# Kernel tuning notes

Measured on AMD Instinct MI355X. Metric: run time of the kernel, lower is better.

The kernel has to match this reference:

```python
import jax, jax.numpy as jnp
import numpy as np

B, C, F, T = 4, 64, 257, 256
H, OUT = 256, 64

def setup_inputs() -> dict:
    key = jax.random.key(0)
    ks = jax.random.split(key, 7)
    w = lambda k, shape: jax.random.normal(k, shape, dtype=jnp.float32) * 0.05
    return {
        "x": jax.random.normal(ks[0], (B, C, F, T), dtype=jnp.float32),
        "W_ih": w(ks[1], (4 * H, C)),   # torch LSTM weight_ih_l0, gate order i,f,g,o
        "W_hh": w(ks[2], (4 * H, H)),   # weight_hh_l0
        "b_ih": w(ks[3], (4 * H,)),
        "b_hh": w(ks[4], (4 * H,)),
        "W_lin": w(ks[5], (OUT, H)),
        "b_lin": w(ks[6], (OUT,)),
    }

def _lstm(y, W_ih, W_hh, b_ih, b_hh):
    # y: (N, T, C) -> (N, T, H); PyTorch gate order i, f, g, o
    N, Tl, _ = y.shape
    Hd = W_hh.shape[1]
    # precompute input contributions for all timesteps in one big GEMM
    x_gates = jnp.einsum('ntc,gc->ntg', y, W_ih) + b_ih + b_hh  # (N, T, 4H)

    def step(carry, xg):
        h, c = carry
        g = xg + h @ W_hh.T  # (N, 4H)
        i, f, gg, o = jnp.split(g, 4, axis=-1)
        c = jax.nn.sigmoid(f) * c + jax.nn.sigmoid(i) * jnp.tanh(gg)
        h = jax.nn.sigmoid(o) * jnp.tanh(c)
        return (h, c), h

    h0 = jnp.zeros((N, Hd), y.dtype)
    _, hs = jax.lax.scan(step, (h0, h0), jnp.swapaxes(x_gates, 0, 1))  # (T, N, H)
    return jnp.swapaxes(hs, 0, 1)  # (N, T, H)

def reference(x, W_ih, W_hh, b_ih, b_hh, W_lin, b_lin):
    b, c, f, t = x.shape
    y = x.transpose(0, 2, 3, 1).reshape(b * f, t, c)  # (B*F, T, C)
    h = _lstm(y, W_ih, W_hh, b_ih, b_hh)              # (B*F, T, H)
    out = h @ W_lin.T + b_lin                          # (B*F, T, OUT)
    return out.reshape(b, f, t, -1).transpose(0, 3, 1, 2)  # (B, OUT, F, T)
```

## Files before the change

### kernel.cpp

```cpp
#include <hip/hip_runtime.h>

#define NSEQ 1028
#define TT   256
#define CC   64
#define HH   256
#define SLABE 32768
#define AROWX 528
#define XG_A  (16*AROWX)
#define XG_LDS (2*XG_A + 2*SLABE*2)
#define AROWB 656
#define FB_LDS (2*16*AROWB + 2*SLABE*2)
#define OUTP_LDS (128*264*2 + 64*264*2)

typedef unsigned short u16;
typedef float  f32x4 __attribute__((ext_vector_type(4)));
typedef __bf16 v8bf  __attribute__((ext_vector_type(8)));

__device__ __forceinline__ u16 f2bf(float f){
  unsigned u = __builtin_bit_cast(unsigned, f);
  u += 0x7FFFu + ((u >> 16) & 1u);
  return (u16)(u >> 16);
}
__device__ __forceinline__ float sigm(float x){
  float t = __builtin_amdgcn_exp2f(-1.4426950408889634f * x);
  return __builtin_amdgcn_rcpf(1.0f + t);
}
__device__ __forceinline__ float tanh_f(float x){
  float a = __builtin_fabsf(x);
  float t = __builtin_amdgcn_exp2f(-2.885390081777927f * a);
  float r = (1.0f - t) * __builtin_amdgcn_rcpf(1.0f + t);
  return __builtin_copysignf(r, x);
}
__device__ __forceinline__ void mfma_a(f32x4& d, v8bf a, v8bf b){
  asm("v_mfma_f32_16x16x32_bf16 %0, %1, %2, %0" : "+v"(d) : "v"(a), "a"(b));
}
__device__ __forceinline__ void mfma_v(f32x4& d, v8bf a, v8bf b){
  asm("v_mfma_f32_16x16x32_bf16 %0, %1, %2, %0" : "+v"(d) : "v"(a), "v"(b));
}

__global__ void k_pack_w(const float* __restrict__ Whh, const float* __restrict__ Wih,
                         u16* __restrict__ wpack){
  int idx = blockIdx.x*256 + threadIdx.x;
  if (idx >= 10*SLABE) return;
  int j    = idx & 7;
  int lane = (idx >> 3) & 63;
  int ct   = (idx >> 9) & 7;
  int w    = (idx >> 12) & 7;
  int kt   = idx >> 15;
  int col  = (ct >> 1)*256 + w*32 + (ct & 1)*16 + (lane & 15);
  int k    = kt*32 + (lane >> 4)*8 + j;
  float v  = (k < 256) ? Whh[col*256 + k] : Wih[col*64 + (k - 256)];
  wpack[idx] = f2bf(v);
}

__global__ void k_bias(const float* __restrict__ bi, const float* __restrict__ bh,
                       float* __restrict__ bias){
  int i = blockIdx.x*256 + threadIdx.x;
  if (i < 1024) bias[i] = bi[i] + bh[i];
}

__global__ void k_wlin(const float* __restrict__ Wl, u16* __restrict__ wlin){
  int i = blockIdx.x*256 + threadIdx.x;
  if (i >= 64*264) return;
  int col = i / 264, k = i % 264;
  wlin[i] = (k < 256) ? f2bf(Wl[col*256 + k]) : (u16)0;
}

__global__ void k_ytrans(const float* __restrict__ x, u16* __restrict__ ybuf){
  __shared__ u16 tile[64][257];
  int n = blockIdx.x, b = n / 257, f = n % 257, tid = threadIdx.x;
  for (int i = tid; i < 64*256; i += 256){
    int c = i >> 8, t = i & 255;
    tile[c][t] = f2bf(x[((size_t)(b*64 + c)*257 + f)*256 + t]);
  }
  __syncthreads();
  for (int i = tid; i < 256*64; i += 256){
    int t = i >> 6, c = i & 63;
    ybuf[((size_t)n*256 + t)*64 + c] = tile[c][t];
  }
}

__global__ __launch_bounds__(512) void k_xgates(const u16* __restrict__ wpack,
      const float* __restrict__ bias, const u16* __restrict__ ybuf,
      u16* __restrict__ xgp){
  __shared__ u16 yt[16*16*72];
  const int g = blockIdx.x, t0 = blockIdx.y*16, n0 = g*16;
  const int tid = threadIdx.x, lane = tid & 63, w = tid >> 6;
  const int l15 = lane & 15, q = lane >> 4;

  v8bf wf[2][8];
  #pragma unroll
  for (int kf = 0; kf < 2; ++kf)
    #pragma unroll
    for (int ct = 0; ct < 8; ++ct)
      wf[kf][ct] = *(const v8bf*)(wpack + (((8 + kf)*8 + w)*8 + ct)*512 + lane*8);
  float biasr[8];
  #pragma unroll
  for (int ct = 0; ct < 8; ++ct)
    biasr[ct] = bias[(ct >> 1)*256 + w*32 + (ct & 1)*16 + l15];

  #pragma unroll
  for (int s = 0; s < 4; ++s){
    int i = tid + s*512;
    int seq = i >> 7, tt = (i >> 3) & 15, c8 = i & 7;
    uint4 v = {0u,0u,0u,0u};
    if (n0 + seq < NSEQ)
      v = *(const uint4*)(ybuf + ((size_t)(n0 + seq)*TT + t0 + tt)*64 + c8*8);
    *(uint4*)(yt + tt*1152 + seq*72 + c8*8) = v;
  }
  __syncthreads();

  for (int tt = 0; tt < 16; ++tt){
    f32x4 acc[8];
    #pragma unroll
    for (int ct = 0; ct < 8; ++ct)
      acc[ct] = (f32x4){biasr[ct], biasr[ct], biasr[ct], biasr[ct]};
    v8bf a0 = *(const v8bf*)(yt + tt*1152 + l15*72 + q*8);
    v8bf a1 = *(const v8bf*)(yt + tt*1152 + l15*72 + 32 + q*8);
    #pragma unroll
    for (int ct = 0; ct < 8; ++ct){
      acc[ct] = __builtin_amdgcn_mfma_f32_16x16x32_bf16(a0, wf[0][ct], acc[ct], 0, 0, 0);
      acc[ct] = __builtin_amdgcn_mfma_f32_16x16x32_bf16(a1, wf[1][ct], acc[ct], 0, 0, 0);
    }
    unsigned dw[16];
    #pragma unroll
    for (int ct = 0; ct < 8; ++ct)
      #pragma unroll
      for (int p = 0; p < 2; ++p)
        dw[ct*2 + p] = (unsigned)f2bf(acc[ct][2*p]) | ((unsigned)f2bf(acc[ct][2*p + 1]) << 16);
    u16* dst = xgp + ((((size_t)g*TT + t0 + tt)*8 + w)*64 + lane)*32;
    *(uint4*)(dst +  0) = (uint4){dw[0], dw[1], dw[2], dw[3]};
    *(uint4*)(dst +  8) = (uint4){dw[4], dw[5], dw[6], dw[7]};
    *(uint4*)(dst + 16) = (uint4){dw[8], dw[9], dw[10], dw[11]};
    *(uint4*)(dst + 24) = (uint4){dw[12], dw[13], dw[14], dw[15]};
  }
}

__global__ __launch_bounds__(512, 2) void k_lstm_xg(const u16* __restrict__ wpack,
      const u16* __restrict__ xgp, u16* __restrict__ hbuf){
  extern __shared__ char smem[];
  char* lA = smem;
  u16*  lW = (u16*)(smem + 2*XG_A);
  const int tid = threadIdx.x, lane = tid & 63, w = tid >> 6;
  const int g = blockIdx.x, n0 = g*16;
  const int l15 = lane & 15, q = lane >> 4;
  const int srow = tid >> 5, schunk = tid & 31;

  v8bf wreg[4][8];
  #pragma unroll
  for (int kt = 0; kt < 4; ++kt)
    #pragma unroll
    for (int ct = 0; ct < 8; ++ct)
      wreg[kt][ct] = *(const v8bf*)(wpack + ((kt*8 + w)*8 + ct)*512 + lane*8);

  {
    const uint4* src = (const uint4*)(wpack + 4*SLABE);
    uint4* dst = (uint4*)lW;
    for (int i = tid; i < (2*SLABE)/8; i += 512) dst[i] = src[i];
  }
  {
    unsigned* z = (unsigned*)lA;
    for (int i = tid; i < (2*XG_A)/4; i += 512) z[i] = 0;
  }
  f32x4 creg[2];
  creg[0] = (f32x4){0.f,0.f,0.f,0.f};
  creg[1] = (f32x4){0.f,0.f,0.f,0.f};
  __syncthreads();

  const u16* wp = wpack;

  v8bf sbuf[8];
  uint4 xgv[4];
  {
    const u16* wpw0 = wp + w*4096 + lane*8;
    #pragma unroll
    for (int ct = 0; ct < 8; ++ct) sbuf[ct] = *(const v8bf*)(wpw0 + 6*SLABE + ct*512);
    const u16* xb = xgp + ((((size_t)g*TT + 0)*8 + w)*64 + lane)*32;
    xgv[0] = *(const uint4*)(xb +  0);
    xgv[1] = *(const uint4*)(xb +  8);
    xgv[2] = *(const uint4*)(xb + 16);
    xgv[3] = *(const uint4*)(xb + 24);
  }

  for (int t = 0; t < TT; ++t){
    char* Acur = lA + (t & 1)*XG_A;
    char* Anxt = lA + ((t + 1) & 1)*XG_A;
    asm("" : "+s"(wp));
    const u16* wpw = wp + w*4096 + lane*8;

    if (t >= 1 && n0 + srow < NSEQ){
      uint4 hv = *(const uint4*)(Acur + srow*AROWX + schunk*16);
      *(uint4*)(hbuf + ((size_t)(n0 + srow)*TT + (t - 1))*HH + schunk*8) = hv;
    }

    f32x4 acc[8];
    #pragma unroll
    for (int ct = 0; ct < 8; ++ct){
      #pragma unroll
      for (int p = 0; p < 2; ++p){
        unsigned u = ((const unsigned*)&xgv[(ct*2 + p) >> 2])[(ct*2 + p) & 3];
        acc[ct][2*p]     = __builtin_bit_cast(float, u << 16);
        acc[ct][2*p + 1] = __builtin_bit_cast(float, u & 0xffff0000u);
      }
    }
    asm volatile("s_nop 1"
      : "+v"(acc[0]), "+v"(acc[1]), "+v"(acc[2]), "+v"(acc[3]),
        "+v"(acc[4]), "+v"(acc[5]), "+v"(acc[6]), "+v"(acc[7]));

    if (t + 1 < TT){
      const u16* xb = xgp + ((((size_t)g*TT + (t + 1))*8 + w)*64 + lane)*32;
      xgv[0] = *(const uint4*)(xb +  0);
      xgv[1] = *(const uint4*)(xb +  8);
      xgv[2] = *(const uint4*)(xb + 16);
      xgv[3] = *(const uint4*)(xb + 24);
    }
    __builtin_amdgcn_sched_barrier(0);

    #define AFRAGX(kt) (*(const v8bf*)(Acur + l15*AROWX + (kt)*64 + q*16))
    #define LFRAGX(kt,ct) (*(const v8bf*)(lW + (((kt)-4)*8 + w)*4096 + (ct)*512 + lane*8))

    { v8bf a = AFRAGX(0);
      #pragma unroll
      for (int ct = 0; ct < 8; ++ct) mfma_a(acc[ct], a, wreg[0][ct]); }
    { v8bf a = AFRAGX(6);
      #pragma unroll
      for (int ct = 0; ct < 8; ++ct) mfma_v(acc[ct], a, sbuf[ct]);
      #pragma unroll
      for (int ct = 0; ct < 8; ++ct) sbuf[ct] = *(const v8bf*)(wpw + 7*SLABE + ct*512);
      __builtin_amdgcn_sched_barrier(0); }
    { v8bf a = AFRAGX(1);
      #pragma unroll
      for (int ct = 0; ct < 8; ++ct) mfma_a(acc[ct], a, wreg[1][ct]); }
    { v8bf a = AFRAGX(2);
      #pragma unroll
      for (int ct = 0; ct < 8; ++ct) mfma_a(acc[ct], a, wreg[2][ct]); }
    { v8bf a = AFRAGX(3);
      #pragma unroll
      for (int ct = 0; ct < 8; ++ct) mfma_a(acc[ct], a, wreg[3][ct]); }
    { v8bf a = AFRAGX(4);
      #pragma unroll
      for (int ct = 0; ct < 8; ++ct) mfma_v(acc[ct], a, LFRAGX(4,ct)); }
    { v8bf a = AFRAGX(7);
      #pragma unroll
      for (int ct = 0; ct < 8; ++ct) mfma_v(acc[ct], a, sbuf[ct]);
      #pragma unroll
      for (int ct = 0; ct < 8; ++ct) sbuf[ct] = *(const v8bf*)(wpw + 6*SLABE + ct*512);
      __builtin_amdgcn_sched_barrier(0); }
    { v8bf a = AFRAGX(5);
      #pragma unroll
      for (int ct = 0; ct < 8; ++ct) mfma_v(acc[ct], a, LFRAGX(5,ct)); }

    asm volatile("s_nop 7\n\ts_nop 7\n\ts_nop 7"
      : "+v"(acc[0]), "+v"(acc[1]), "+v"(acc[2]), "+v"(acc[3]),
        "+v"(acc[4]), "+v"(acc[5]), "+v"(acc[6]), "+v"(acc[7]));

    #pragma unroll
    for (int u = 0; u < 2; ++u){
      #pragma unroll
      for (int j = 0; j < 4; ++j){
        float xi = acc[0 + u][j], xf = acc[2 + u][j], xg = acc[4 + u][j], xo = acc[6 + u][j];
        float cv = sigm(xf)*creg[u][j] + sigm(xi)*tanh_f(xg);
        float hv = sigm(xo)*tanh_f(cv);
        creg[u][j] = cv;
        int row = 4*q + j, unit = w*32 + u*16 + l15;
        *(u16*)(Anxt + row*AROWX + unit*2) = f2bf(hv);
      }
    }
    __syncthreads();
  }
  {
    char* Afin = lA + (TT & 1)*XG_A;
    if (n0 + srow < NSEQ){
      uint4 hv = *(const uint4*)(Afin + srow*AROWX + schunk*16);
      *(uint4*)(hbuf + ((size_t)(n0 + srow)*TT + (TT - 1))*HH + schunk*8) = hv;
    }
  }
}

__global__ __launch_bounds__(512, 2) void k_lstm_fb(const u16* __restrict__ wpack,
      const float* __restrict__ bias, const u16* __restrict__ ybuf,
      u16* __restrict__ hbuf){
  extern __shared__ char smem[];
  char* lA = smem;
  u16*  lW = (u16*)(smem + 2*16*AROWB);
  const int tid = threadIdx.x, lane = tid & 63, w = tid >> 6;
  const int n0 = blockIdx.x * 16;
  const int l15 = lane & 15, q = lane >> 4;
  const int srow = tid >> 5, schunk = tid & 31;

  v8bf wreg[4][8];
  #pragma unroll
  for (int kt = 0; kt < 4; ++kt)
    #pragma unroll
    for (int ct = 0; ct < 8; ++ct)
      wreg[kt][ct] = *(const v8bf*)(wpack + ((kt*8 + w)*8 + ct)*512 + lane*8);
  {
    const uint4* src = (const uint4*)(wpack + 4*SLABE);
    uint4* dst = (uint4*)lW;
    for (int i = tid; i < (2*SLABE)/8; i += 512) dst[i] = src[i];
  }
  float biasr[8];
  #pragma unroll
  for (int ct = 0; ct < 8; ++ct)
    biasr[ct] = bias[(ct >> 1)*256 + w*32 + (ct & 1)*16 + l15];
  {
    unsigned* z = (unsigned*)lA;
    for (int i = tid; i < (2*16*AROWB)/4; i += 512) z[i] = 0;
  }
  __syncthreads();
  {
    unsigned v = 0;
    if (n0 + srow < NSEQ)
      v = *(const unsigned*)(ybuf + ((size_t)(n0 + srow)*TT + 0)*64 + (tid & 31)*2);
    *(unsigned*)(lA + srow*AROWB + 512 + (tid & 31)*4) = v;
  }
  f32x4 creg[2];
  creg[0] = (f32x4){0.f,0.f,0.f,0.f};
  creg[1] = (f32x4){0.f,0.f,0.f,0.f};
  __syncthreads();

  const u16* wp = wpack;
  v8bf sbuf[8];
  {
    const u16* wpw0 = wp + w*4096 + lane*8;
    #pragma unroll
    for (int ct = 0; ct < 8; ++ct) sbuf[ct] = *(const v8bf*)(wpw0 + 6*SLABE + ct*512);
  }

  for (int t = 0; t < TT; ++t){
    char* Acur = lA + (t & 1)*16*AROWB;
    char* Anxt = lA + ((t + 1) & 1)*16*AROWB;
    asm("" : "+s"(wp));
    const u16* wpw = wp + w*4096 + lane*8;

    unsigned yv = 0;
    if (t + 1 < TT && n0 + srow < NSEQ)
      yv = *(const unsigned*)(ybuf + ((size_t)(n0 + srow)*TT + (t + 1))*64 + (tid & 31)*2);

    if (t >= 1 && n0 + srow < NSEQ){
      uint4 hv = *(const uint4*)(Acur + srow*AROWB + schunk*16);
      *(uint4*)(hbuf + ((size_t)(n0 + srow)*TT + (t - 1))*HH + schunk*8) = hv;
    }

    f32x4 acc[8];
    #pragma unroll
    for (int ct = 0; ct < 8; ++ct)
      acc[ct] = (f32x4){biasr[ct], biasr[ct], biasr[ct], biasr[ct]};
    asm volatile("s_nop 1"
      : "+v"(acc[0]), "+v"(acc[1]), "+v"(acc[2]), "+v"(acc[3]),
        "+v"(acc[4]), "+v"(acc[5]), "+v"(acc[6]), "+v"(acc[7]));

    #define AFRAG(kt) (*(const v8bf*)(Acur + l15*AROWB + (kt)*64 + q*16))
    #define LFRAG(kt,ct) (*(const v8bf*)(lW + (((kt)-4)*8 + w)*4096 + (ct)*512 + lane*8))

    { v8bf a = AFRAG(0);
      #pragma unroll
      for (int ct = 0; ct < 8; ++ct) mfma_a(acc[ct], a, wreg[0][ct]); }
    { v8bf a = AFRAG(1);
      #pragma unroll
      for (int ct = 0; ct < 8; ++ct) mfma_a(acc[ct], a, wreg[1][ct]); }
    { v8bf a = AFRAG(6);
      #pragma unroll
      for (int ct = 0; ct < 8; ++ct) mfma_v(acc[ct], a, sbuf[ct]);
      #pragma unroll
      for (int ct = 0; ct < 8; ++ct) sbuf[ct] = *(const v8bf*)(wpw + 7*SLABE + ct*512);
      __builtin_amdgcn_sched_barrier(0); }
    { v8bf a = AFRAG(2);
      #pragma unroll
      for (int ct = 0; ct < 8; ++ct) mfma_a(acc[ct], a, wreg[2][ct]); }
    { v8bf a = AFRAG(3);
      #pragma unroll
      for (int ct = 0; ct < 8; ++ct) mfma_a(acc[ct], a, wreg[3][ct]); }
    { v8bf a = AFRAG(7);
      #pragma unroll
      for (int ct = 0; ct < 8; ++ct) mfma_v(acc[ct], a, sbuf[ct]);
      #pragma unroll
      for (int ct = 0; ct < 8; ++ct) sbuf[ct] = *(const v8bf*)(wpw + 8*SLABE + ct*512);
      __builtin_amdgcn_sched_barrier(0); }
    { v8bf a = AFRAG(4);
      #pragma unroll
      for (int ct = 0; ct < 8; ++ct) mfma_v(acc[ct], a, LFRAG(4,ct)); }
    { v8bf a = AFRAG(8);
      #pragma unroll
      for (int ct = 0; ct < 8; ++ct) mfma_v(acc[ct], a, sbuf[ct]);
      #pragma unroll
      for (int ct = 0; ct < 8; ++ct) sbuf[ct] = *(const v8bf*)(wpw + 9*SLABE + ct*512);
      __builtin_amdgcn_sched_barrier(0); }
    { v8bf a = AFRAG(5);
      #pragma unroll
      for (int ct = 0; ct < 8; ++ct) mfma_v(acc[ct], a, LFRAG(5,ct)); }
    { v8bf a = AFRAG(9);
      #pragma unroll
      for (int ct = 0; ct < 8; ++ct) mfma_v(acc[ct], a, sbuf[ct]);
      #pragma unroll
      for (int ct = 0; ct < 8; ++ct) sbuf[ct] = *(const v8bf*)(wpw + 6*SLABE + ct*512);
      __builtin_amdgcn_sched_barrier(0); }

    asm volatile("s_nop 7\n\ts_nop 7\n\ts_nop 7"
      : "+v"(acc[0]), "+v"(acc[1]), "+v"(acc[2]), "+v"(acc[3]),
        "+v"(acc[4]), "+v"(acc[5]), "+v"(acc[6]), "+v"(acc[7]));

    #pragma unroll
    for (int u = 0; u < 2; ++u){
      #pragma unroll
      for (int j = 0; j < 4; ++j){
        float xi = acc[0 + u][j], xf = acc[2 + u][j], xg = acc[4 + u][j], xo = acc[6 + u][j];
        float cv = sigm(xf)*creg[u][j] + sigm(xi)*tanh_f(xg);
        float hv = sigm(xo)*tanh_f(cv);
        creg[u][j] = cv;
        int row = 4*q + j, unit = w*32 + u*16 + l15;
        *(u16*)(Anxt + row*AROWB + unit*2) = f2bf(hv);
      }
    }
    if (t + 1 < TT)
      *(unsigned*)(Anxt + srow*AROWB + 512 + (tid & 31)*4) = yv;
    __syncthreads();
  }
  {
    char* Afin = lA + (TT & 1)*16*AROWB;
    if (n0 + srow < NSEQ){
      uint4 hv = *(const uint4*)(Afin + srow*AROWB + schunk*16);
      *(uint4*)(hbuf + ((size_t)(n0 + srow)*TT + (TT - 1))*HH + schunk*8) = hv;
    }
  }
}

__global__ __launch_bounds__(256) void k_outproj(const u16* __restrict__ hbuf,
      const u16* __restrict__ wlin, const float* __restrict__ blin,
      float* __restrict__ out){
  extern __shared__ char smem[];
  u16* sA = (u16*)smem;
  u16* sB = (u16*)(smem + 128*264*2);
  const int n = blockIdx.x, th = blockIdx.y, t0 = th*128;
  const int b = n / 257, f = n % 257;
  const int tid = threadIdx.x, lane = tid & 63, wv = tid >> 6;

  for (int i = tid; i < 128*32; i += 256){
    int r = i >> 5, part = i & 31;
    *(uint4*)(sA + r*264 + part*8) =
        *(const uint4*)(hbuf + ((size_t)n*TT + t0 + r)*HH + part*8);
  }
  for (int i = tid; i < (64*264)/2; i += 256)
    ((unsigned*)sB)[i] = ((const unsigned*)wlin)[i];
  __syncthreads();

  f32x4 acc[2][4];
  #pragma unroll
  for (int m = 0; m < 2; ++m)
    #pragma unroll
    for (int nt = 0; nt < 4; ++nt){
      float bv = blin[nt*16 + (lane & 15)];
      acc[m][nt] = (f32x4){bv, bv, bv, bv};
    }
  const int khi = (lane >> 4) * 8;
  #pragma unroll
  for (int kt = 0; kt < 8; ++kt){
    v8bf av[2];
    #pragma unroll
    for (int m = 0; m < 2; ++m){
      int mt = wv*2 + m;
      av[m] = *(const v8bf*)(sA + (mt*16 + (lane & 15))*264 + kt*32 + khi);
    }
    #pragma unroll
    for (int nt = 0; nt < 4; ++nt){
      v8bf bv = *(const v8bf*)(sB + (nt*16 + (lane & 15))*264 + kt*32 + khi);
      #pragma unroll
      for (int m = 0; m < 2; ++m)
        acc[m][nt] = __builtin_amdgcn_mfma_f32_16x16x32_bf16(av[m], bv, acc[m][nt], 0, 0, 0);
    }
  }
  #pragma unroll
  for (int m = 0; m < 2; ++m){
    int mt = wv*2 + m;
    #pragma unroll
    for (int nt = 0; nt < 4; ++nt){
      int o = nt*16 + (lane & 15);
      int tb = t0 + mt*16 + 4*(lane >> 4);
      *(f32x4*)(out + (((size_t)b*64 + o)*257 + f)*TT + tb) = acc[m][nt];
    }
  }
}

extern "C" void kernel_launch(void* const* d_in, const int* in_sizes, int n_in,
                              void* d_out, int out_size, void* d_ws, size_t ws_size,
                              hipStream_t stream) {
  const float* x   = (const float*)d_in[0];
  const float* Wih = (const float*)d_in[1];
  const float* Whh = (const float*)d_in[2];
  const float* bih = (const float*)d_in[3];
  const float* bhh = (const float*)d_in[4];
  const float* Wl  = (const float*)d_in[5];
  const float* bl  = (const float*)d_in[6];
  float* out = (float*)d_out;

  char* p = (char*)d_ws;
  u16*   wpack = (u16*)p;   p += 655360;
  float* bias  = (float*)p; p += 4096;
  u16*   wlin  = (u16*)p;   p += 33792;
  u16*   ybuf  = (u16*)p;   p += (size_t)NSEQ*TT*CC*2;
  u16*   hbuf  = (u16*)p;   p += (size_t)NSEQ*TT*HH*2;
  u16*   xgp   = (u16*)p;
  const size_t XGP_BYTES = (size_t)65*TT*8*64*32*2;
  const size_t NEED = (size_t)(p - (char*)d_ws) + XGP_BYTES;

  hipFuncSetAttribute((const void*)k_lstm_xg, hipFuncAttributeMaxDynamicSharedMemorySize, XG_LDS);
  hipFuncSetAttribute((const void*)k_lstm_fb, hipFuncAttributeMaxDynamicSharedMemorySize, FB_LDS);
  hipFuncSetAttribute((const void*)k_outproj, hipFuncAttributeMaxDynamicSharedMemorySize, OUTP_LDS);

  k_pack_w <<<1280, 256, 0, stream>>>(Whh, Wih, wpack);
  k_bias   <<<4,    256, 0, stream>>>(bih, bhh, bias);
  k_wlin   <<<66,   256, 0, stream>>>(Wl, wlin);
  k_ytrans <<<1028, 256, 0, stream>>>(x, ybuf);

  if (ws_size >= NEED) {
    k_xgates <<<dim3(65, 16), 512, 0, stream>>>(wpack, bias, ybuf, xgp);
    k_lstm_xg<<<65, 512, XG_LDS, stream>>>(wpack, xgp, hbuf);
  } else {
    k_lstm_fb<<<65, 512, FB_LDS, stream>>>(wpack, bias, ybuf, hbuf);
  }
  k_outproj<<<dim3(1028, 2), 256, OUTP_LDS, stream>>>(hbuf, wlin, bl, out);
}
```

Baseline: 1.199 ms.

## Chunk LSTM time loop to fit precomputed input gates in workspace

Splits the time dimension into chunks whose size depends on available workspace. Each chunk launches an input-gate GEMM then the recurrent kernel, with hidden and cell state carried across launches via global buffers. This lets the precomputed-input-gates path run when the full buffer doesn't fit, instead of the fallback kernel. It also replaces __syncthreads with an LDS-only wait barrier and reorders MFMA k-tiles. The cost is extra launches and state save/restore per chunk.

```diff
diff --git a/kernel.cpp b/kernel.cpp
--- a/kernel.cpp
+++ b/kernel.cpp
@@ -5,8 +5,8 @@
 #define CC   64
 #define HH   256
 #define SLABE 32768
-#define AROWX 528
-#define XG_A  (16*AROWX)
+#define XROW 528
+#define XG_A (16*XROW)
 #define XG_LDS (2*XG_A + 2*SLABE*2)
 #define AROWB 656
 #define FB_LDS (2*16*AROWB + 2*SLABE*2)
@@ -36,6 +36,12 @@
 }
 __device__ __forceinline__ void mfma_v(f32x4& d, v8bf a, v8bf b){
   asm("v_mfma_f32_16x16x32_bf16 %0, %1, %2, %0" : "+v"(d) : "v"(a), "v"(b));
+}
+__device__ __forceinline__ void soft_barrier(){
+  asm volatile("s_waitcnt lgkmcnt(0)" ::: "memory");
+  __builtin_amdgcn_sched_barrier(0);
+  __builtin_amdgcn_s_barrier();
+  __builtin_amdgcn_sched_barrier(0);
 }
 
 __global__ void k_pack_w(const float* __restrict__ Whh, const float* __restrict__ Wih,
@@ -82,9 +88,9 @@
 
 __global__ __launch_bounds__(512) void k_xgates(const u16* __restrict__ wpack,
       const float* __restrict__ bias, const u16* __restrict__ ybuf,
-      u16* __restrict__ xgp){
+      u16* __restrict__ xgs, int t0, int CH){
   __shared__ u16 yt[16*16*72];
-  const int g = blockIdx.x, t0 = blockIdx.y*16, n0 = g*16;
+  const int g = blockIdx.x, tb = blockIdx.y*16, n0 = g*16;
   const int tid = threadIdx.x, lane = tid & 63, w = tid >> 6;
   const int l15 = lane & 15, q = lane >> 4;
 
@@ -105,7 +111,7 @@
     int seq = i >> 7, tt = (i >> 3) & 15, c8 = i & 7;
     uint4 v = {0u,0u,0u,0u};
     if (n0 + seq < NSEQ)
-      v = *(const uint4*)(ybuf + ((size_t)(n0 + seq)*TT + t0 + tt)*64 + c8*8);
+      v = *(const uint4*)(ybuf + ((size_t)(n0 + seq)*TT + t0 + tb + tt)*64 + c8*8);
     *(uint4*)(yt + tt*1152 + seq*72 + c8*8) = v;
   }
   __syncthreads();
@@ -128,7 +134,7 @@
       #pragma unroll
       for (int p = 0; p < 2; ++p)
         dw[ct*2 + p] = (unsigned)f2bf(acc[ct][2*p]) | ((unsigned)f2bf(acc[ct][2*p + 1]) << 16);
-    u16* dst = xgp + ((((size_t)g*TT + t0 + tt)*8 + w)*64 + lane)*32;
+    u16* dst = xgs + ((((size_t)g*CH + tb + tt)*8 + w)*64 + lane)*32;
     *(uint4*)(dst +  0) = (uint4){dw[0], dw[1], dw[2], dw[3]};
     *(uint4*)(dst +  8) = (uint4){dw[4], dw[5], dw[6], dw[7]};
     *(uint4*)(dst + 16) = (uint4){dw[8], dw[9], dw[10], dw[11]};
@@ -137,7 +143,8 @@
 }
 
 __global__ __launch_bounds__(512, 2) void k_lstm_xg(const u16* __restrict__ wpack,
-      const u16* __restrict__ xgp, u16* __restrict__ hbuf){
+      const u16* __restrict__ xgs, u16* __restrict__ hbuf, float* __restrict__ cbuf,
+      int t0, int CH){
   extern __shared__ char smem[];
   char* lA = smem;
   u16*  lW = (u16*)(smem + 2*XG_A);
@@ -152,19 +159,29 @@
     #pragma unroll
     for (int ct = 0; ct < 8; ++ct)
       wreg[kt][ct] = *(const v8bf*)(wpack + ((kt*8 + w)*8 + ct)*512 + lane*8);
-
   {
     const uint4* src = (const uint4*)(wpack + 4*SLABE);
     uint4* dst = (uint4*)lW;
     for (int i = tid; i < (2*SLABE)/8; i += 512) dst[i] = src[i];
   }
   {
-    unsigned* z = (unsigned*)lA;
-    for (int i = tid; i < (2*XG_A)/4; i += 512) z[i] = 0;
+    uint4 hv = {0u,0u,0u,0u};
+    if (t0 > 0 && n0 + srow < NSEQ)
+      hv = *(const uint4*)(hbuf + ((size_t)(n0 + srow)*TT + (t0 - 1))*HH + schunk*8);
+    *(uint4*)(lA + (t0 & 1)*XG_A + srow*XROW + schunk*16) = hv;
   }
   f32x4 creg[2];
   creg[0] = (f32x4){0.f,0.f,0.f,0.f};
   creg[1] = (f32x4){0.f,0.f,0.f,0.f};
+  if (t0 > 0){
+    #pragma unroll
+    for (int u = 0; u < 2; ++u)
+      #pragma unroll
+      for (int j = 0; j < 4; ++j){
+        int row = 4*q + j, unit = w*32 + u*16 + l15;
+        if (n0 + row < NSEQ) creg[u][j] = cbuf[(size_t)(n0 + row)*HH + unit];
+      }
+  }
   __syncthreads();
 
   const u16* wp = wpack;
@@ -175,21 +192,21 @@
     const u16* wpw0 = wp + w*4096 + lane*8;
     #pragma unroll
     for (int ct = 0; ct < 8; ++ct) sbuf[ct] = *(const v8bf*)(wpw0 + 6*SLABE + ct*512);
-    const u16* xb = xgp + ((((size_t)g*TT + 0)*8 + w)*64 + lane)*32;
+    const u16* xb = xgs + ((((size_t)g*CH + 0)*8 + w)*64 + lane)*32;
     xgv[0] = *(const uint4*)(xb +  0);
     xgv[1] = *(const uint4*)(xb +  8);
     xgv[2] = *(const uint4*)(xb + 16);
     xgv[3] = *(const uint4*)(xb + 24);
   }
 
-  for (int t = 0; t < TT; ++t){
+  for (int t = t0; t < t0 + CH; ++t){
     char* Acur = lA + (t & 1)*XG_A;
     char* Anxt = lA + ((t + 1) & 1)*XG_A;
     asm("" : "+s"(wp));
     const u16* wpw = wp + w*4096 + lane*8;
 
-    if (t >= 1 && n0 + srow < NSEQ){
-      uint4 hv = *(const uint4*)(Acur + srow*AROWX + schunk*16);
+    if (t > t0 && n0 + srow < NSEQ){
+      uint4 hv = *(const uint4*)(Acur + srow*XROW + schunk*16);
       *(uint4*)(hbuf + ((size_t)(n0 + srow)*TT + (t - 1))*HH + schunk*8) = hv;
     }
 
@@ -207,8 +224,8 @@
       : "+v"(acc[0]), "+v"(acc[1]), "+v"(acc[2]), "+v"(acc[3]),
         "+v"(acc[4]), "+v"(acc[5]), "+v"(acc[6]), "+v"(acc[7]));
 
-    if (t + 1 < TT){
-      const u16* xb = xgp + ((((size_t)g*TT + (t + 1))*8 + w)*64 + lane)*32;
+    if (t + 1 < t0 + CH){
+      const u16* xb = xgs + ((((size_t)g*CH + (t + 1 - t0))*8 + w)*64 + lane)*32;
       xgv[0] = *(const uint4*)(xb +  0);
       xgv[1] = *(const uint4*)(xb +  8);
       xgv[2] = *(const uint4*)(xb + 16);
@@ -216,18 +233,18 @@
     }
     __builtin_amdgcn_sched_barrier(0);
 
-    #define AFRAGX(kt) (*(const v8bf*)(Acur + l15*AROWX + (kt)*64 + q*16))
+    #define AFRAGX(kt) (*(const v8bf*)(Acur + l15*XROW + (kt)*64 + q*16))
     #define LFRAGX(kt,ct) (*(const v8bf*)(lW + (((kt)-4)*8 + w)*4096 + (ct)*512 + lane*8))
 
-    { v8bf a = AFRAGX(0);
-      #pragma unroll
-      for (int ct = 0; ct < 8; ++ct) mfma_a(acc[ct], a, wreg[0][ct]); }
     { v8bf a = AFRAGX(6);
       #pragma unroll
       for (int ct = 0; ct < 8; ++ct) mfma_v(acc[ct], a, sbuf[ct]);
       #pragma unroll
       for (int ct = 0; ct < 8; ++ct) sbuf[ct] = *(const v8bf*)(wpw + 7*SLABE + ct*512);
       __builtin_amdgcn_sched_barrier(0); }
+    { v8bf a = AFRAGX(0);
+      #pragma unroll
+      for (int ct = 0; ct < 8; ++ct) mfma_a(acc[ct], a, wreg[0][ct]); }
     { v8bf a = AFRAGX(1);
       #pragma unroll
       for (int ct = 0; ct < 8; ++ct) mfma_a(acc[ct], a, wreg[1][ct]); }
@@ -240,15 +257,15 @@
     { v8bf a = AFRAGX(4);
       #pragma unroll
       for (int ct = 0; ct < 8; ++ct) mfma_v(acc[ct], a, LFRAGX(4,ct)); }
+    { v8bf a = AFRAGX(5);
+      #pragma unroll
+      for (int ct = 0; ct < 8; ++ct) mfma_v(acc[ct], a, LFRAGX(5,ct)); }
     { v8bf a = AFRAGX(7);
       #pragma unroll
       for (int ct = 0; ct < 8; ++ct) mfma_v(acc[ct], a, sbuf[ct]);
       #pragma unroll
       for (int ct = 0; ct < 8; ++ct) sbuf[ct] = *(const v8bf*)(wpw + 6*SLABE + ct*512);
       __builtin_amdgcn_sched_barrier(0); }
-    { v8bf a = AFRAGX(5);
-      #pragma unroll
-      for (int ct = 0; ct < 8; ++ct) mfma_v(acc[ct], a, LFRAGX(5,ct)); }
 
     asm volatile("s_nop 7\n\ts_nop 7\n\ts_nop 7"
       : "+v"(acc[0]), "+v"(acc[1]), "+v"(acc[2]), "+v"(acc[3]),
@@ -263,17 +280,24 @@
         float hv = sigm(xo)*tanh_f(cv);
         creg[u][j] = cv;
         int row = 4*q + j, unit = w*32 + u*16 + l15;
-        *(u16*)(Anxt + row*AROWX + unit*2) = f2bf(hv);
+        *(u16*)(Anxt + row*XROW + unit*2) = f2bf(hv);
       }
     }
-    __syncthreads();
-  }
-  {
-    char* Afin = lA + (TT & 1)*XG_A;
+    soft_barrier();
+  }
+  {
+    char* Afin = lA + ((t0 + CH) & 1)*XG_A;
     if (n0 + srow < NSEQ){
-      uint4 hv = *(const uint4*)(Afin + srow*AROWX + schunk*16);
-      *(uint4*)(hbuf + ((size_t)(n0 + srow)*TT + (TT - 1))*HH + schunk*8) = hv;
-    }
+      uint4 hv = *(const uint4*)(Afin + srow*XROW + schunk*16);
+      *(uint4*)(hbuf + ((size_t)(n0 + srow)*TT + (t0 + CH - 1))*HH + schunk*8) = hv;
+    }
+    #pragma unroll
+    for (int u = 0; u < 2; ++u)
+      #pragma unroll
+      for (int j = 0; j < 4; ++j){
+        int row = 4*q + j, unit = w*32 + u*16 + l15;
+        if (n0 + row < NSEQ) cbuf[(size_t)(n0 + row)*HH + unit] = creg[u][j];
+      }
   }
 }
 
@@ -311,8 +335,8 @@
   {
     unsigned v = 0;
     if (n0 + srow < NSEQ)
-      v = *(const unsigned*)(ybuf + ((size_t)(n0 + srow)*TT + 0)*64 + (tid & 31)*2);
-    *(unsigned*)(lA + srow*AROWB + 512 + (tid & 31)*4) = v;
+      v = *(const unsigned*)(ybuf + ((size_t)(n0 + srow)*TT + 0)*64 + schunk*2);
+    *(unsigned*)(lA + srow*AROWB + 512 + schunk*4) = v;
   }
   f32x4 creg[2];
   creg[0] = (f32x4){0.f,0.f,0.f,0.f};
@@ -335,7 +359,7 @@
 
     unsigned yv = 0;
     if (t + 1 < TT && n0 + srow < NSEQ)
-      yv = *(const unsigned*)(ybuf + ((size_t)(n0 + srow)*TT + (t + 1))*64 + (tid & 31)*2);
+      yv = *(const unsigned*)(ybuf + ((size_t)(n0 + srow)*TT + (t + 1))*64 + schunk*2);
 
     if (t >= 1 && n0 + srow < NSEQ){
       uint4 hv = *(const uint4*)(Acur + srow*AROWB + schunk*16);
@@ -413,8 +437,8 @@
       }
     }
     if (t + 1 < TT)
-      *(unsigned*)(Anxt + srow*AROWB + 512 + (tid & 31)*4) = yv;
-    __syncthreads();
+      *(unsigned*)(Anxt + srow*AROWB + 512 + schunk*4) = yv;
+    soft_barrier();
   }
   {
     char* Afin = lA + (TT & 1)*16*AROWB;
@@ -497,11 +521,16 @@
   u16*   wpack = (u16*)p;   p += 655360;
   float* bias  = (float*)p; p += 4096;
   u16*   wlin  = (u16*)p;   p += 33792;
+  float* cbuf  = (float*)p; p += (size_t)NSEQ*HH*4;
   u16*   ybuf  = (u16*)p;   p += (size_t)NSEQ*TT*CC*2;
   u16*   hbuf  = (u16*)p;   p += (size_t)NSEQ*TT*HH*2;
-  u16*   xgp   = (u16*)p;
-  const size_t XGP_BYTES = (size_t)65*TT*8*64*32*2;
-  const size_t NEED = (size_t)(p - (char*)d_ws) + XGP_BYTES;
+  u16*   xgs   = (u16*)p;
+  const size_t BASE = (size_t)(p - (char*)d_ws);
+
+  int CH = 0;
+  if      (ws_size >= BASE + 65ull*64*32768) CH = 64;
+  else if (ws_size >= BASE + 65ull*32*32768) CH = 32;
+  else if (ws_size >= BASE + 65ull*16*32768) CH = 16;
 
   hipFuncSetAttribute((const void*)k_lstm_xg, hipFuncAttributeMaxDynamicSharedMemorySize, XG_LDS);
   hipFuncSetAttribute((const void*)k_lstm_fb, hipFuncAttributeMaxDynamicSharedMemorySize, FB_LDS);
@@ -512,9 +541,11 @@
   k_wlin   <<<66,   256, 0, stream>>>(Wl, wlin);
   k_ytrans <<<1028, 256, 0, stream>>>(x, ybuf);
 
-  if (ws_size >= NEED) {
-    k_xgates <<<dim3(65, 16), 512, 0, stream>>>(wpack, bias, ybuf, xgp);
-    k_lstm_xg<<<65, 512, XG_LDS, stream>>>(wpack, xgp, hbuf);
+  if (CH) {
+    for (int t0 = 0; t0 < TT; t0 += CH){
+      k_xgates <<<dim3(65, CH/16), 512, 0, stream>>>(wpack, bias, ybuf, xgs, t0, CH);
+      k_lstm_xg<<<65, 512, XG_LDS, stream>>>(wpack, xgs, hbuf, cbuf, t0, CH);
+    }
   } else {
     k_lstm_fb<<<65, 512, FB_LDS, stream>>>(wpack, bias, ybuf, hbuf);
   }
```

Measured after the change: 1.263 ms. +5.4%, slower.
